# Optimization experiments

Measured on AMD Instinct MI355X. Metric: run time of the kernel, lower is better.

Reference implementation:

```python
import jax, jax.numpy as jnp
import numpy as np

B, S, H, I, E, K = 2, 1024, 768, 1536, 8, 2
CAPACITY_FACTOR = 1.5
ROUTING_TEMP = 1.0
LB_WEIGHT = 0.001


def setup_inputs() -> dict:
    key = jax.random.key(0)
    k_x, k_g, k_w1, k_w3, k_w2 = jax.random.split(key, 5)
    std = 0.02
    return {
        "x": jax.random.normal(k_x, (B, S, H), dtype=jnp.float32),
        "w_gate": jax.random.normal(k_g, (H, E), dtype=jnp.float32) * 0.02,
        "w1": jax.random.normal(k_w1, (E, H, I), dtype=jnp.float32) * std,
        "w3": jax.random.normal(k_w3, (E, H, I), dtype=jnp.float32) * std,
        "w2": jax.random.normal(k_w2, (E, I, H), dtype=jnp.float32) * (std / np.sqrt(2 * 12)),
    }


def _moe_forward(x, w_gate, w1, w3, w2):
    Bb, Ss, Hh = x.shape
    T = Bb * Ss
    xf = x.reshape(T, Hh)

    # --- routing ---
    gate_logits = (xf @ w_gate) / ROUTING_TEMP          # [T, E]
    gate_probs = jax.nn.softmax(gate_logits, axis=-1)   # [T, E]
    topk_probs, topk_idx = jax.lax.top_k(gate_probs, K)  # [T, K]
    topk_probs = topk_probs / (topk_probs.sum(-1, keepdims=True) + 1e-8)

    # --- capacity dropping (per-k slot, token order, like the torch loop) ---
    capacity = max(8, int((T * K // E) * CAPACITY_FACTOR))
    onehot = (topk_idx[:, :, None] == jnp.arange(E)[None, None, :])  # [T, K, E] bool
    ranks = jnp.cumsum(onehot.astype(jnp.int32), axis=0)             # position of token in expert queue
    keep = onehot & (ranks <= capacity)                               # [T, K, E]

    # combine weight per (token, expert): sum over k of kept, clamped routing prob
    w_clamped = jnp.clip(topk_probs, 1e-8, 10.0)                      # [T, K]
    combine = jnp.einsum("tk,tke->te", w_clamped, keep.astype(xf.dtype))  # [T, E]

    # --- dense per-expert SwiGLU (reference form of masked dispatch) ---
    g = jnp.einsum("th,ehi->tei", xf, w1)   # [T, E, I]
    u = jnp.einsum("th,ehi->tei", xf, w3)   # [T, E, I]
    h = jax.nn.silu(g) * u                    # [T, E, I]
    y = jnp.einsum("tei,eih->teh", h, w2)   # [T, E, H]
    out = jnp.einsum("te,teh->th", combine, y).reshape(Bb, Ss, Hh)

    # --- load balancing loss ---
    expert_counts = keep.sum(axis=(0, 1)).astype(jnp.float32)         # [E]
    dropped = (onehot.sum() - keep.sum()).astype(jnp.float32)
    expert_usage = jax.lax.stop_gradient(expert_counts) / float(max(T * K, 1))
    gate_importance = gate_probs.mean(axis=0)                          # [E]
    aux = jnp.sum(expert_usage * gate_importance) * E
    aux = aux + jnp.where(dropped > 0, dropped / float(max(T, 1)) * 0.1, 0.0)
    aux = jnp.minimum(aux, 1.0) * LB_WEIGHT
    return out, aux


def reference(x, w_gate, w1, w3, w2):
    return _moe_forward(x, w_gate, w1, w3, w2)
```

## Files before the change

### kernel.cpp

```cpp
#include <hip/hip_runtime.h>
#include <math.h>

#define T_TOK 2048
#define HD 768
#define ID 1536
#define NE 8
#define CAP 768
#define TK 4096
#define RT 12
#define NB1 24
#define KC1 24
#define NB2 12
#define KC2 48
#define W2BLK 576

typedef __bf16 bf16_t;
typedef __bf16 bf16x8 __attribute__((ext_vector_type(8)));
typedef __bf16 bf16x4 __attribute__((ext_vector_type(4)));
typedef float floatx4 __attribute__((ext_vector_type(4)));

__device__ __forceinline__ void gld16(const bf16_t* g, bf16_t* l) {
  __builtin_amdgcn_global_load_lds(
      (__attribute__((address_space(1))) void*)(g),
      (__attribute__((address_space(3))) void*)(l),
      16, 0, 0);
}

__device__ __forceinline__ unsigned short bfbits(float f) {
  union { bf16_t b; unsigned short u; } c;
  c.b = (bf16_t)f;
  return c.u;
}

__device__ __forceinline__ void rp_load(const float* __restrict__ src, int C,
                                        int kc, int t256, unsigned* T32) {
  int r = t256 >> 3, c0 = (t256 & 7) * 8;
  const float* sp = src + (size_t)(kc * 32 + r) * C + c0;
  float4 v0 = *(const float4*)sp;
  float4 v1 = *(const float4*)(sp + 4);
  float f[8] = {v0.x, v0.y, v0.z, v0.w, v1.x, v1.y, v1.z, v1.w};
  unsigned* tb = T32 + r * 33 + (c0 >> 1);
#pragma unroll
  for (int k = 0; k < 4; ++k)
    tb[k] = (unsigned)bfbits(f[2 * k]) | ((unsigned)bfbits(f[2 * k + 1]) << 16);
}

__device__ __forceinline__ void rp_store(bf16_t* __restrict__ dst, int kc,
                                         int t256, const unsigned* T32) {
  int n = t256 >> 2, p4 = t256 & 3;
  int c8 = p4 ^ ((n >> 1) & 3);
  int half = n & 1, nh = n >> 1;
  unsigned short u[8];
#pragma unroll
  for (int j = 0; j < 8; ++j) {
    unsigned w = T32[(c8 * 8 + j) * 33 + nh];
    u[j] = half ? (unsigned short)(w >> 16) : (unsigned short)(w & 0xffffu);
  }
  uint4 o;
  o.x = (unsigned)u[0] | ((unsigned)u[1] << 16);
  o.y = (unsigned)u[2] | ((unsigned)u[3] << 16);
  o.z = (unsigned)u[4] | ((unsigned)u[5] << 16);
  o.w = (unsigned)u[6] | ((unsigned)u[7] << 16);
  *(uint4*)(dst + (size_t)kc * 2048 + t256 * 8) = o;
}

__global__ void k_route(const float* __restrict__ x, const float* __restrict__ wg,
                        bf16_t* __restrict__ xbf, int2* __restrict__ idx2,
                        float2* __restrict__ wc2, float* __restrict__ probs8) {
  int b = blockIdx.x;
  int tid = threadIdx.x;
  int t = b * 4 + (tid >> 6);
  int lane = tid & 63;
  const float* xr = x + (size_t)t * HD;
  int off = lane * 12;
  float4 a = *(const float4*)(xr + off);
  float4 bv = *(const float4*)(xr + off + 4);
  float4 c = *(const float4*)(xr + off + 8);
  float xv[12] = {a.x, a.y, a.z, a.w, bv.x, bv.y, bv.z, bv.w, c.x, c.y, c.z, c.w};
  bf16x4 s0, s1, s2;
#pragma unroll
  for (int j = 0; j < 4; ++j) { s0[j] = (bf16_t)xv[j]; s1[j] = (bf16_t)xv[4 + j]; s2[j] = (bf16_t)xv[8 + j]; }
  bf16_t* xo = xbf + (size_t)t * HD + off;
  *(bf16x4*)xo = s0; *(bf16x4*)(xo + 4) = s1; *(bf16x4*)(xo + 8) = s2;

  float acc[8] = {0, 0, 0, 0, 0, 0, 0, 0};
#pragma unroll
  for (int jj = 0; jj < 12; ++jj) {
    const float4* wr = (const float4*)(wg + (size_t)(off + jj) * 8);
    float4 w0 = wr[0], w1v = wr[1];
    float v = xv[jj];
    acc[0] += v * w0.x; acc[1] += v * w0.y; acc[2] += v * w0.z; acc[3] += v * w0.w;
    acc[4] += v * w1v.x; acc[5] += v * w1v.y; acc[6] += v * w1v.z; acc[7] += v * w1v.w;
  }
#pragma unroll
  for (int e = 0; e < 8; ++e) {
    float v = acc[e];
    for (int s = 1; s < 64; s <<= 1) v += __shfl_xor(v, s, 64);
    acc[e] = v;
  }
  float mx = acc[0];
#pragma unroll
  for (int e = 1; e < 8; ++e) mx = fmaxf(mx, acc[e]);
  float p[8], sum = 0.f;
#pragma unroll
  for (int e = 0; e < 8; ++e) { p[e] = __expf(acc[e] - mx); sum += p[e]; }
#pragma unroll
  for (int e = 0; e < 8; ++e) p[e] /= sum;
  if (lane == 0) {
    float4 P0 = make_float4(p[0], p[1], p[2], p[3]);
    float4 P1 = make_float4(p[4], p[5], p[6], p[7]);
    *(float4*)&probs8[t * 8] = P0;
    *(float4*)&probs8[t * 8 + 4] = P1;
    int e0 = 0;
#pragma unroll
    for (int e = 1; e < 8; ++e) if (p[e] > p[e0]) e0 = e;
    int e1 = (e0 == 0) ? 1 : 0;
#pragma unroll
    for (int e = 0; e < 8; ++e) if (e != e0 && p[e] > p[e1]) e1 = e;
    float denom = p[e0] + p[e1] + 1e-8f;
    float w0c = fminf(fmaxf(p[e0] / denom, 1e-8f), 10.f);
    float w1c = fminf(fmaxf(p[e1] / denom, 1e-8f), 10.f);
    idx2[t] = make_int2(e0, e1);
    wc2[t] = make_float2(w0c, w1c);
  }
}

__global__ void k_scan(const int2* __restrict__ idx2, const float2* __restrict__ wc2,
                       const float* __restrict__ probs8,
                       const float* __restrict__ w1, const float* __restrict__ w3,
                       bf16_t* __restrict__ w1b, bf16_t* __restrict__ w3b,
                       int* __restrict__ tok_of_row, int2* __restrict__ rows2,
                       int2* __restrict__ cnt_start, float* __restrict__ aux_out) {
  __shared__ unsigned sTr[4 * 2 * 1056];
  if (blockIdx.x > 0) {
    int rb = blockIdx.x - 1;
    int m = rb >= 576;
    int r3 = m ? rb - 576 : rb;
    int pan = r3 / 3;
    int kc0 = (r3 - pan * 3) * 8;
    int e = pan & 7, nb = pan >> 3;
    const float* src = (m ? w3 : w1) + (size_t)e * HD * ID + nb * 64;
    bf16_t* dst = (m ? w3b : w1b) + (size_t)(e * NB1 + nb) * (KC1 * 2048);
    int grp = threadIdx.x >> 8, lt = threadIdx.x & 255;
    unsigned* T0 = sTr + grp * 2 * 1056;
    unsigned* T1 = T0 + 1056;
    int kc = kc0 + grp * 2;
    rp_load(src, ID, kc, lt, T0);
    __syncthreads();
    rp_load(src, ID, kc + 1, lt, T1);
    rp_store(dst, kc, lt, T0);
    __syncthreads();
    rp_store(dst, kc + 1, lt, T1);
    return;
  }
  __shared__ int2 sIdx[2048];
  __shared__ int sTot[16];
  __shared__ int sPos[8];
  __shared__ float sImp[16][8];
  int tid = threadIdx.x;
  sIdx[tid] = idx2[tid]; sIdx[tid + 1024] = idx2[tid + 1024];
  rows2[tid] = make_int2(-1, -1); rows2[tid + 1024] = make_int2(-1, -1);
  const float4* pp = (const float4*)probs8;
  float4 u0 = pp[tid * 4], u1 = pp[tid * 4 + 1], u2 = pp[tid * 4 + 2], u3 = pp[tid * 4 + 3];
  float im[8] = {u0.x + u2.x, u0.y + u2.y, u0.z + u2.z, u0.w + u2.w,
                 u1.x + u3.x, u1.y + u3.y, u1.z + u3.z, u1.w + u3.w};
#pragma unroll
  for (int e = 0; e < 8; ++e) {
    float v = im[e];
    for (int d = 1; d < 64; d <<= 1) v += __shfl_xor(v, d, 64);
    im[e] = v;
  }
  int w = tid >> 6, lane = tid & 63;
  if (lane == 0) {
#pragma unroll
    for (int e = 0; e < 8; ++e) sImp[w][e] = im[e];
  }
  __syncthreads();
  int s = w >> 3, e = w & 7;
  int t0 = lane * 32;
  int cnt = 0;
  for (int j = 0; j < 32; ++j) {
    int2 p = sIdx[t0 + j];
    cnt += ((s ? p.y : p.x) == e) ? 1 : 0;
  }
  int incl = cnt;
  for (int d = 1; d < 64; d <<= 1) {
    int v = __shfl_up(incl, d, 64);
    if (lane >= d) incl += v;
  }
  int excl = incl - cnt;
  if (lane == 63) sTot[w] = incl;
  __syncthreads();
  if (tid == 0) {
    int run = 0; float a = 0.f;
    for (int ee = 0; ee < 8; ++ee) {
      float impv = 0.f;
      for (int ww = 0; ww < 16; ++ww) impv += sImp[ww][ee];
      int k = min(sTot[ee], CAP) + min(sTot[8 + ee], CAP);
      sPos[ee] = run;
      cnt_start[ee] = make_int2(run, k);
      a += ((float)k / (float)TK) * (impv / (float)T_TOK);
      run += k;
    }
    a *= (float)NE;
    int dropped = TK - run;
    if (dropped > 0) a += (float)dropped / (float)T_TOK * 0.1f;
    aux_out[0] = fminf(a, 1.f) * 0.001f;
  }
  __syncthreads();
  int rank = excl;
  for (int j = 0; j < 32; ++j) {
    int t = t0 + j;
    int2 p = sIdx[t];
    int ex = s ? p.y : p.x;
    if (ex == e) {
      rank++;
      if (rank <= CAP) {
        int pos = atomicAdd(&sPos[e], 1);
        tok_of_row[pos] = t;
        ((int*)rows2)[2 * t + s] = pos;
      }
    }
  }
}

__global__ __launch_bounds__(256, 4)
void k_gemm1(const bf16_t* __restrict__ xbf, const bf16_t* __restrict__ w1b,
             const bf16_t* __restrict__ w3b, const float* __restrict__ w2,
             bf16_t* __restrict__ w2b, const int* __restrict__ tok_of_row,
             const int2* __restrict__ cnt_start, bf16_t* __restrict__ h_ws) {
  __shared__ __attribute__((aligned(16))) bf16_t Abuf[128 * 32];
  __shared__ __attribute__((aligned(16))) bf16_t B1buf[64 * 32];
  __shared__ __attribute__((aligned(16))) bf16_t B3buf[64 * 32];
  __shared__ unsigned Trp[2 * 1056];
  if (blockIdx.x < W2BLK) {
    int q = blockIdx.x;
    int pan = q / 6;
    int kc0 = (q - pan * 6) * 8;
    int e = pan & 7, nb = pan >> 3;
    const float* src = w2 + (size_t)e * ID * HD + nb * 64;
    bf16_t* dst = w2b + (size_t)(e * NB2 + nb) * (KC2 * 2048);
    int tid = threadIdx.x;
    rp_load(src, HD, kc0, tid, Trp);
    for (int t = 0; t < 8; ++t) {
      __syncthreads();
      if (t < 7) rp_load(src, HD, kc0 + t + 1, tid, Trp + ((t + 1) & 1) * 1056);
      rp_store(dst, kc0 + t, tid, Trp + (t & 1) * 1056);
    }
    return;
  }
  int bx = blockIdx.x - W2BLK;
  int e = bx & 7;
  int t = bx >> 3;
  int nb = t / RT, rt = t - nb * RT;
  int2 cs = cnt_start[e];
  int nrows = cs.y - rt * 128;
  if (nrows <= 0) return;
  if (nrows > 128) nrows = 128;
  int grow0 = cs.x + rt * 128;

  int tid = threadIdx.x;
  int lane = tid & 63, wv = tid >> 6;
  int wm = wv & 1, wn = wv >> 1;
  int lr = lane & 15, q = lane >> 4;
  int rdc = (q ^ ((lane >> 1) & 3)) * 8;
  int srow = lane >> 2;
  int gch = ((lane & 3) ^ ((lane >> 3) & 3)) * 8;

  int ra = wv * 32 + srow;
  int tokA0 = tok_of_row[grow0 + min(ra, nrows - 1)];
  int tokA1 = tok_of_row[grow0 + min(ra + 16, nrows - 1)];
  const bf16_t* gA0 = xbf + (size_t)tokA0 * HD + gch;
  const bf16_t* gA1 = xbf + (size_t)tokA1 * HD + gch;
  const bf16_t* p1 = w1b + (size_t)((e * NB1 + nb) * KC1) * 2048 + tid * 8;
  const bf16_t* p3 = w3b + (size_t)((e * NB1 + nb) * KC1) * 2048 + tid * 8;
  bf16_t* lA0 = &Abuf[(wv * 32) * 32];
  bf16_t* lA1 = &Abuf[(wv * 32 + 16) * 32];
  bf16_t* lB1 = &B1buf[wv * 512];
  bf16_t* lB3 = &B3buf[wv * 512];

  floatx4 accg[4][2] = {};
  floatx4 accu[4][2] = {};

  for (int kk = 0; kk < KC1; ++kk) {
    __syncthreads();
    gld16(gA0, lA0); gld16(gA1, lA1);
    gld16(p1, lB1); gld16(p3, lB3);
    gA0 += 32; gA1 += 32; p1 += 2048; p3 += 2048;
    __syncthreads();
    bf16x8 af[4], b1f[2], b3f[2];
#pragma unroll
    for (int i = 0; i < 4; ++i) af[i] = *(const bf16x8*)&Abuf[(wm * 64 + i * 16 + lr) * 32 + rdc];
#pragma unroll
    for (int i = 0; i < 2; ++i) b1f[i] = *(const bf16x8*)&B1buf[(wn * 32 + i * 16 + lr) * 32 + rdc];
#pragma unroll
    for (int i = 0; i < 2; ++i) b3f[i] = *(const bf16x8*)&B3buf[(wn * 32 + i * 16 + lr) * 32 + rdc];
#pragma unroll
    for (int i = 0; i < 4; ++i)
#pragma unroll
      for (int jj = 0; jj < 2; ++jj) {
        accg[i][jj] = __builtin_amdgcn_mfma_f32_16x16x32_bf16(af[i], b1f[jj], accg[i][jj], 0, 0, 0);
        accu[i][jj] = __builtin_amdgcn_mfma_f32_16x16x32_bf16(af[i], b3f[jj], accu[i][jj], 0, 0, 0);
      }
  }
#pragma unroll
  for (int i = 0; i < 4; ++i)
#pragma unroll
    for (int r = 0; r < 4; ++r) {
      int rl = wm * 64 + i * 16 + q * 4 + r;
      if (rl < nrows) {
        size_t rb = (size_t)(grow0 + rl) * ID + nb * 64 + wn * 32 + lr;
#pragma unroll
        for (int jj = 0; jj < 2; ++jj) {
          float gg = accg[i][jj][r], uu = accu[i][jj][r];
          float sg = gg / (1.f + __expf(-gg));
          h_ws[rb + jj * 16] = (bf16_t)(sg * uu);
        }
      }
    }
}

__global__ __launch_bounds__(256, 4)
void k_gemm2(const bf16_t* __restrict__ h_ws, const bf16_t* __restrict__ w2b,
             const int2* __restrict__ cnt_start, float* __restrict__ y) {
  int e = blockIdx.x & 7;
  int t = blockIdx.x >> 3;
  int nb = t / RT, rt = t - nb * RT;
  int2 cs = cnt_start[e];
  int nrows = cs.y - rt * 128;
  if (nrows <= 0) return;
  if (nrows > 128) nrows = 128;
  int grow0 = cs.x + rt * 128;

  __shared__ __attribute__((aligned(16))) bf16_t Abuf[128 * 32];
  __shared__ __attribute__((aligned(16))) bf16_t Bbuf[64 * 32];

  int tid = threadIdx.x;
  int lane = tid & 63, wv = tid >> 6;
  int wm = wv & 1, wn = wv >> 1;
  int lr = lane & 15, q = lane >> 4;
  int rdc = (q ^ ((lane >> 1) & 3)) * 8;
  int srow = lane >> 2;
  int gch = ((lane & 3) ^ ((lane >> 3) & 3)) * 8;

  int ra = wv * 32 + srow;
  const bf16_t* gA0 = h_ws + (size_t)(grow0 + min(ra, nrows - 1)) * ID + gch;
  const bf16_t* gA1 = h_ws + (size_t)(grow0 + min(ra + 16, nrows - 1)) * ID + gch;
  const bf16_t* pB = w2b + (size_t)((e * NB2 + nb) * KC2) * 2048 + tid * 8;
  bf16_t* lA0 = &Abuf[(wv * 32) * 32];
  bf16_t* lA1 = &Abuf[(wv * 32 + 16) * 32];
  bf16_t* lB = &Bbuf[wv * 512];

  floatx4 acc[4][2] = {};

  for (int kk = 0; kk < KC2; ++kk) {
    __syncthreads();
    gld16(gA0, lA0); gld16(gA1, lA1);
    gld16(pB, lB);
    gA0 += 32; gA1 += 32; pB += 2048;
    __syncthreads();
    bf16x8 af[4], bfr[2];
#pragma unroll
    for (int i = 0; i < 4; ++i) af[i] = *(const bf16x8*)&Abuf[(wm * 64 + i * 16 + lr) * 32 + rdc];
#pragma unroll
    for (int i = 0; i < 2; ++i) bfr[i] = *(const bf16x8*)&Bbuf[(wn * 32 + i * 16 + lr) * 32 + rdc];
#pragma unroll
    for (int i = 0; i < 4; ++i)
#pragma unroll
      for (int jj = 0; jj < 2; ++jj)
        acc[i][jj] = __builtin_amdgcn_mfma_f32_16x16x32_bf16(af[i], bfr[jj], acc[i][jj], 0, 0, 0);
  }
#pragma unroll
  for (int i = 0; i < 4; ++i)
#pragma unroll
    for (int r = 0; r < 4; ++r) {
      int rl = wm * 64 + i * 16 + q * 4 + r;
      if (rl < nrows) {
        size_t ob = (size_t)(grow0 + rl) * HD + nb * 64 + wn * 32 + lr;
#pragma unroll
        for (int jj = 0; jj < 2; ++jj)
          y[ob + jj * 16] = acc[i][jj][r];
      }
    }
}

__global__ void k_comb(const float* __restrict__ y, const int2* __restrict__ rows2,
                       const float2* __restrict__ wc2, float* __restrict__ out) {
  int tid = threadIdx.x;
  int t = blockIdx.x * 4 + (tid >> 6);
  int lane = tid & 63;
  int2 r = rows2[t];
  float2 w = wc2[t];
  int off = lane * 12;
  floatx4 o0 = {0.f, 0.f, 0.f, 0.f}, o1 = o0, o2 = o0;
  if (r.x >= 0) {
    const float* yr = y + (size_t)r.x * HD + off;
    floatx4 a = *(const floatx4*)(yr);
    floatx4 b = *(const floatx4*)(yr + 4);
    floatx4 c = *(const floatx4*)(yr + 8);
    o0 += w.x * a; o1 += w.x * b; o2 += w.x * c;
  }
  if (r.y >= 0) {
    const float* yr = y + (size_t)r.y * HD + off;
    floatx4 a = *(const floatx4*)(yr);
    floatx4 b = *(const floatx4*)(yr + 4);
    floatx4 c = *(const floatx4*)(yr + 8);
    o0 += w.y * a; o1 += w.y * b; o2 += w.y * c;
  }
  float* op = out + (size_t)t * HD + off;
  *(floatx4*)(op) = o0;
  *(floatx4*)(op + 4) = o1;
  *(floatx4*)(op + 8) = o2;
}

extern "C" void kernel_launch(void* const* d_in, const int* in_sizes, int n_in,
                              void* d_out, int out_size, void* d_ws, size_t ws_size,
                              hipStream_t stream) {
  const float* x  = (const float*)d_in[0];
  const float* wg = (const float*)d_in[1];
  const float* w1 = (const float*)d_in[2];
  const float* w3 = (const float*)d_in[3];
  const float* w2 = (const float*)d_in[4];
  float* out = (float*)d_out;

  char* ws = (char*)d_ws;
  bf16_t* xbf  = (bf16_t*)(ws + 0);
  bf16_t* w1b  = (bf16_t*)(ws + 3145728);
  bf16_t* w3b  = (bf16_t*)(ws + 22020096);
  bf16_t* w2b  = (bf16_t*)(ws + 40894464);
  bf16_t* h_ws = (bf16_t*)(ws + 59768832);
  float*  probs8     = (float*)(ws + 72351744);
  int2*   idx2       = (int2*)(ws + 72417280);
  float2* wc2        = (float2*)(ws + 72433664);
  int*    tok_of_row = (int*)(ws + 72450048);
  int2*   rows2      = (int2*)(ws + 72466432);
  int2*   cnt_start  = (int2*)(ws + 72482816);
  float*  y_ws = (float*)(ws + 3145728);

  float* aux_out = out + (size_t)T_TOK * HD;

  k_route<<<512, 256, 0, stream>>>(x, wg, xbf, idx2, wc2, probs8);
  k_scan<<<1 + 1152, 1024, 0, stream>>>(idx2, wc2, probs8, w1, w3, w1b, w3b,
                                        tok_of_row, rows2, cnt_start, aux_out);
  k_gemm1<<<W2BLK + 8 * NB1 * RT, 256, 0, stream>>>(xbf, w1b, w3b, w2, w2b,
                                                    tok_of_row, cnt_start, h_ws);
  k_gemm2<<<8 * NB2 * RT, 256, 0, stream>>>(h_ws, w2b, cnt_start, y_ws);
  k_comb<<<512, 256, 0, stream>>>(y_ws, rows2, wc2, out);
}
```

Baseline: 231.5 us.

## Fuse expert combine into second GEMM epilogue via weighted atomic adds

Removes the separate combine kernel and the intermediate y buffer. The output is zeroed inside the routing kernel, and k_gemm2 now scatters weight-scaled results directly into the output rows of each token with float atomicAdd, using per-row token ids and routing weights recorded during the scan. This saves a launch and a full write plus read of y, but adds atomic traffic and makes the summation order nondeterministic.

```diff
diff --git a/kernel.cpp b/kernel.cpp
--- a/kernel.cpp
+++ b/kernel.cpp
@@ -66,9 +66,15 @@
 
 __global__ void k_route(const float* __restrict__ x, const float* __restrict__ wg,
                         bf16_t* __restrict__ xbf, int2* __restrict__ idx2,
-                        float2* __restrict__ wc2, float* __restrict__ probs8) {
+                        float2* __restrict__ wc2, float* __restrict__ probs8,
+                        float* __restrict__ outz) {
   int b = blockIdx.x;
   int tid = threadIdx.x;
+#pragma unroll
+  for (int k2 = 0; k2 < 3; ++k2) {
+    float4 z = make_float4(0.f, 0.f, 0.f, 0.f);
+    *(float4*)(outz + (size_t)b * 3072 + k2 * 1024 + tid * 4) = z;
+  }
   int t = b * 4 + (tid >> 6);
   int lane = tid & 63;
   const float* xr = x + (size_t)t * HD;
@@ -129,7 +135,7 @@
                        const float* __restrict__ probs8,
                        const float* __restrict__ w1, const float* __restrict__ w3,
                        bf16_t* __restrict__ w1b, bf16_t* __restrict__ w3b,
-                       int* __restrict__ tok_of_row, int2* __restrict__ rows2,
+                       int* __restrict__ tok_of_row, float* __restrict__ wgt_of_row,
                        int2* __restrict__ cnt_start, float* __restrict__ aux_out) {
   __shared__ unsigned sTr[4 * 2 * 1056];
   if (blockIdx.x > 0) {
@@ -159,7 +165,6 @@
   __shared__ float sImp[16][8];
   int tid = threadIdx.x;
   sIdx[tid] = idx2[tid]; sIdx[tid + 1024] = idx2[tid + 1024];
-  rows2[tid] = make_int2(-1, -1); rows2[tid + 1024] = make_int2(-1, -1);
   const float4* pp = (const float4*)probs8;
   float4 u0 = pp[tid * 4], u1 = pp[tid * 4 + 1], u2 = pp[tid * 4 + 2], u3 = pp[tid * 4 + 3];
   float im[8] = {u0.x + u2.x, u0.y + u2.y, u0.z + u2.z, u0.w + u2.w,
@@ -218,7 +223,8 @@
       if (rank <= CAP) {
         int pos = atomicAdd(&sPos[e], 1);
         tok_of_row[pos] = t;
-        ((int*)rows2)[2 * t + s] = pos;
+        float2 wv = wc2[t];
+        wgt_of_row[pos] = s ? wv.y : wv.x;
       }
     }
   }
@@ -322,7 +328,8 @@
 
 __global__ __launch_bounds__(256, 4)
 void k_gemm2(const bf16_t* __restrict__ h_ws, const bf16_t* __restrict__ w2b,
-             const int2* __restrict__ cnt_start, float* __restrict__ y) {
+             const int* __restrict__ tok_of_row, const float* __restrict__ wgt_of_row,
+             const int2* __restrict__ cnt_start, float* __restrict__ out) {
   int e = blockIdx.x & 7;
   int t = blockIdx.x >> 3;
   int nb = t / RT, rt = t - nb * RT;
@@ -376,41 +383,15 @@
     for (int r = 0; r < 4; ++r) {
       int rl = wm * 64 + i * 16 + q * 4 + r;
       if (rl < nrows) {
-        size_t ob = (size_t)(grow0 + rl) * HD + nb * 64 + wn * 32 + lr;
+        int grow = grow0 + rl;
+        int tok = tok_of_row[grow];
+        float wgt = wgt_of_row[grow];
+        size_t ob = (size_t)tok * HD + nb * 64 + wn * 32 + lr;
 #pragma unroll
         for (int jj = 0; jj < 2; ++jj)
-          y[ob + jj * 16] = acc[i][jj][r];
+          atomicAdd(&out[ob + jj * 16], wgt * acc[i][jj][r]);
       }
     }
-}
-
-__global__ void k_comb(const float* __restrict__ y, const int2* __restrict__ rows2,
-                       const float2* __restrict__ wc2, float* __restrict__ out) {
-  int tid = threadIdx.x;
-  int t = blockIdx.x * 4 + (tid >> 6);
-  int lane = tid & 63;
-  int2 r = rows2[t];
-  float2 w = wc2[t];
-  int off = lane * 12;
-  floatx4 o0 = {0.f, 0.f, 0.f, 0.f}, o1 = o0, o2 = o0;
-  if (r.x >= 0) {
-    const float* yr = y + (size_t)r.x * HD + off;
-    floatx4 a = *(const floatx4*)(yr);
-    floatx4 b = *(const floatx4*)(yr + 4);
-    floatx4 c = *(const floatx4*)(yr + 8);
-    o0 += w.x * a; o1 += w.x * b; o2 += w.x * c;
-  }
-  if (r.y >= 0) {
-    const float* yr = y + (size_t)r.y * HD + off;
-    floatx4 a = *(const floatx4*)(yr);
-    floatx4 b = *(const floatx4*)(yr + 4);
-    floatx4 c = *(const floatx4*)(yr + 8);
-    o0 += w.y * a; o1 += w.y * b; o2 += w.y * c;
-  }
-  float* op = out + (size_t)t * HD + off;
-  *(floatx4*)(op) = o0;
-  *(floatx4*)(op + 4) = o1;
-  *(floatx4*)(op + 8) = o2;
 }
 
 extern "C" void kernel_launch(void* const* d_in, const int* in_sizes, int n_in,
@@ -433,17 +414,16 @@
   int2*   idx2       = (int2*)(ws + 72417280);
   float2* wc2        = (float2*)(ws + 72433664);
   int*    tok_of_row = (int*)(ws + 72450048);
-  int2*   rows2      = (int2*)(ws + 72466432);
+  float*  wgt_of_row = (float*)(ws + 72466432);
   int2*   cnt_start  = (int2*)(ws + 72482816);
-  float*  y_ws = (float*)(ws + 3145728);
 
   float* aux_out = out + (size_t)T_TOK * HD;
 
-  k_route<<<512, 256, 0, stream>>>(x, wg, xbf, idx2, wc2, probs8);
+  k_route<<<512, 256, 0, stream>>>(x, wg, xbf, idx2, wc2, probs8, out);
   k_scan<<<1 + 1152, 1024, 0, stream>>>(idx2, wc2, probs8, w1, w3, w1b, w3b,
-                                        tok_of_row, rows2, cnt_start, aux_out);
+                                        tok_of_row, wgt_of_row, cnt_start, aux_out);
   k_gemm1<<<W2BLK + 8 * NB1 * RT, 256, 0, stream>>>(xbf, w1b, w3b, w2, w2b,
                                                     tok_of_row, cnt_start, h_ws);
-  k_gemm2<<<8 * NB2 * RT, 256, 0, stream>>>(h_ws, w2b, cnt_start, y_ws);
-  k_comb<<<512, 256, 0, stream>>>(y_ws, rows2, wc2, out);
-}
+  k_gemm2<<<8 * NB2 * RT, 256, 0, stream>>>(h_ws, w2b, tok_of_row, wgt_of_row,
+                                            cnt_start, out);
+}
```

Measured after the change: 238.1 us. 2.8% more time.
